# Kernel optimization log

Hardware: AMD Instinct MI355X
Metric: run time of the kernel (lower is better)

## Reference

```python
import jax, jax.numpy as jnp
import numpy as np

N_SAMPLES = 4_000_000
N_BUCKETS = 16
K_BASE = 32
K_ADJ = 16


def setup_inputs() -> dict:
    key = jax.random.key(0)
    ks = jax.random.split(key, 8)
    return {
        "x": jax.random.uniform(ks[0], (N_SAMPLES,), dtype=jnp.float32),
        "x_mins": jnp.zeros((N_BUCKETS,), jnp.float32),
        "x_maxs": jnp.ones((N_BUCKETS,), jnp.float32),
        "clip_los": jnp.zeros((N_BUCKETS,), jnp.float32),
        "clip_his": jnp.ones((N_BUCKETS,), jnp.float32),
        "base_knots": jax.random.uniform(ks[1], (K_BASE,), dtype=jnp.float32),
        "base_raw_w": jax.random.normal(ks[2], (K_BASE,), dtype=jnp.float32),
        "base_bias": jax.random.normal(ks[3], (1,), dtype=jnp.float32),
        "adj_knots": jax.random.uniform(ks[4], (K_ADJ,), dtype=jnp.float32),
        "adj_raw_w": jax.random.normal(ks[5], (N_BUCKETS, K_ADJ), dtype=jnp.float32),
        "adj_bias": jax.random.normal(ks[6], (N_BUCKETS,), dtype=jnp.float32),
        "bucket_idx": jax.random.randint(ks[7], (N_SAMPLES,), 0, N_BUCKETS, dtype=jnp.int64),
    }


def _clip_and_scale(x, x_min, x_max, clip_lo, clip_hi):
    # per-sample clip (NaN clip bound => no clipping), then scale to [0,1]
    xc = jnp.where(jnp.isfinite(clip_lo), jnp.maximum(x, clip_lo), x)
    xc = jnp.where(jnp.isfinite(clip_hi), jnp.minimum(xc, clip_hi), xc)
    return jnp.clip((xc - x_min) / (x_max - x_min + 1e-12), 0.0, 1.0)


def _concave_hinge(x01, knots, raw_w, bias):
    # concave, monotone-increasing piecewise-linear spline:
    # f(x) = bias + sum_k softplus(raw_w_k) * min(x, knot_k)
    w = jax.nn.softplus(raw_w)                      # nonneg slopes -> concave increasing
    basis = jnp.minimum(x01[:, None], knots)        # [N, K]
    return bias + jnp.sum(basis * w, axis=-1)       # [N] (w may be [N,K] for per-bucket)


def reference(x, x_mins, x_maxs, clip_los, clip_his, base_knots, base_raw_w,
              base_bias, adj_knots, adj_raw_w, adj_bias, bucket_idx):
    b = bucket_idx.reshape(-1)
    xf = x.reshape(-1)
    # gather per-sample bucket scaling params (replaces the python bucket loop)
    x01 = _clip_and_scale(xf, x_mins[b], x_maxs[b], clip_los[b], clip_his[b])  # [N]
    base = _concave_hinge(x01, base_knots, base_raw_w, base_bias[0])           # [N]
    # vectorized gather-compute in place of unique()+mask dispatch
    adj = _concave_hinge(x01, adj_knots, adj_raw_w[b], adj_bias[b])            # [N]
    return (base + adj)[:, None]                                               # [N,1]
```

## Files before the change

### kernel.cpp

```cpp
#include <hip/hip_runtime.h>
#include <math.h>

#define NB 16
#define KB 32
#define KA 16
#define G  128
#define GP1 (G + 1)
#define LUT_E (NB * GP1)
#define ITERS 4


__device__ __forceinline__ float softplus_f(float v) {
    return fmaxf(v, 0.0f) + log1pf(expf(-fabsf(v)));
}

__global__ __launch_bounds__(256) void build_lut_kernel(
    const float* __restrict__ x_mins,
    const float* __restrict__ x_maxs,
    const float* __restrict__ clip_los,
    const float* __restrict__ clip_his,
    const float* __restrict__ base_knots,
    const float* __restrict__ base_raw_w,
    const float* __restrict__ base_bias,
    const float* __restrict__ adj_knots,
    const float* __restrict__ adj_raw_w,
    const float* __restrict__ adj_bias,
    float* __restrict__ ws)
{
    __shared__ float s_bw[KB], s_bk[KB], s_aw[KA], s_ak[KA];
    __shared__ float s_x0[NB], s_x1[NB];
    __shared__ float s_prm[4];
    __shared__ float s_f[GP1];

    const int tid = threadIdx.x;
    const int b   = blockIdx.x;

    if (tid < KB) { s_bw[tid] = softplus_f(base_raw_w[tid]); s_bk[tid] = base_knots[tid]; }
    if (tid < KA) { s_aw[tid] = softplus_f(adj_raw_w[b * KA + tid]); s_ak[tid] = adj_knots[tid]; }
    if (tid < NB) {
        const float mn = x_mins[tid], mx = x_maxs[tid];
        const float inva = mx - mn + 1e-12f;
        const float a = 1.0f / inva;
        const float c = -mn * a;
        const float lo = clip_los[tid], hi = clip_his[tid];
        const float Lb = isfinite(lo) ? fminf(fmaxf(fmaf(lo, a, c), 0.0f), 1.0f) : 0.0f;
        const float Hb = isfinite(hi) ? fmaxf(fminf(fmaf(hi, a, c), 1.0f), 0.0f) : 1.0f;
        const float x0 = fmaf(Lb, inva, mn);
        const float x1 = fmaf(Hb, inva, mn);
        s_x0[tid] = fminf(x0, x1);
        s_x1[tid] = fmaxf(x0, x1);
        if (tid == b) { s_prm[0] = a; s_prm[1] = c; s_prm[2] = Lb; s_prm[3] = Hb; }
    }
    __syncthreads();

    float xlo = s_x0[0], xhi = s_x1[0];
    #pragma unroll
    for (int i = 1; i < NB; ++i) { xlo = fminf(xlo, s_x0[i]); xhi = fmaxf(xhi, s_x1[i]); }
    if (!(xhi > xlo)) xhi = xlo + 1.0f;
    const float ginv  = (float)G / (xhi - xlo);
    const float hstep = (xhi - xlo) * (1.0f / (float)G);

    if (b == 0 && tid == 0) {
        ws[0] = xlo; ws[1] = ginv; ws[2] = xhi; ws[3] = xlo * ginv;
    }

    if (tid < GP1) {
        const float xj = fmaf(hstep, (float)tid, xlo);
        const float v = fminf(fmaxf(fmaf(xj, s_prm[0], s_prm[1]), s_prm[2]), s_prm[3]);
        float f = adj_bias[b] + base_bias[0];
        #pragma unroll 8
        for (int k = 0; k < KB; ++k)
            f = fmaf(s_bw[k], fminf(v, s_bk[k]), f);
        #pragma unroll 8
        for (int k = 0; k < KA; ++k)
            f = fmaf(s_aw[k], fminf(v, s_ak[k]), f);
        s_f[tid] = f;
    }
    __syncthreads();

    if (tid < GP1) {
        const int jc = min(tid, G - 1);
        const float fl = s_f[jc], fr = s_f[jc + 1];
        const float c1 = (fr - fl) * ginv;
        const float xj = fmaf(hstep, (float)jc, xlo);
        const float c0 = fmaf(-c1, xj, fl);
        ((float2*)(ws + 64))[b * GP1 + tid] = make_float2(c0, c1);
    }
}

__global__ __launch_bounds__(256) void BucketAdjustedHinge_kernel(
    const float* __restrict__ x,
    const int*   __restrict__ bucket_idx,
    const float* __restrict__ ws,
    float*       __restrict__ out,
    int n)
{
    __shared__ float2 s_lut[LUT_E];

    const int tid = threadIdx.x;
    const int gsz = gridDim.x * blockDim.x;
    const int t   = blockIdx.x * blockDim.x + tid;
    const int n4  = n >> 2;

    const float4* __restrict__ x4v = (const float4*)x;
    const int4*   __restrict__ b4v = (const int4*)bucket_idx;
    float4*       __restrict__ o4v = (float4*)out;

    float4 xa[ITERS]; int4 ba[ITERS];
    #pragma unroll
    for (int k = 0; k < ITERS; ++k) {
        const int idx = t + k * gsz;
        if (idx < n4) { xa[k] = x4v[idx]; ba[k] = b4v[idx]; }
    }

    const float xlo  = ws[0];
    const float ginv = ws[1];
    const float xhi  = ws[2];
    const float xlg  = ws[3];

    {
        const float4* __restrict__ src = (const float4*)(ws + 64);
        float4* __restrict__ dst = (float4*)s_lut;
        #pragma unroll
        for (int i = 0; i < 5; ++i) {
            const int j = tid + i * 256;
            if (j < LUT_E / 2) dst[j] = src[j];
        }
    }
    __syncthreads();

    #define EVAL1(xr, b, dstf)                                             \
        {                                                                  \
            const float xc = fminf(fmaxf((xr), xlo), xhi);                 \
            const float tt = fmaf(xc, ginv, -xlg);                         \
            const int cell = min((int)tt, G - 1);                          \
            const float2 cf = s_lut[(b) * GP1 + cell];                     \
            (dstf) = fmaf(xc, cf.y, cf.x);                                 \
        }

    #pragma unroll
    for (int k = 0; k < ITERS; ++k) {
        const int idx = t + k * gsz;
        if (idx < n4) {
            float4 r;
            EVAL1(xa[k].x, ba[k].x, r.x); EVAL1(xa[k].y, ba[k].y, r.y);
            EVAL1(xa[k].z, ba[k].z, r.z); EVAL1(xa[k].w, ba[k].w, r.w);
            o4v[idx] = r;
        }
    }

    for (int idx = t + ITERS * gsz; idx < n4; idx += gsz) {
        const float4 xv = x4v[idx];
        const int4   bv = b4v[idx];
        float4 r;
        EVAL1(xv.x, bv.x, r.x); EVAL1(xv.y, bv.y, r.y);
        EVAL1(xv.z, bv.z, r.z); EVAL1(xv.w, bv.w, r.w);
        o4v[idx] = r;
    }
    for (int i = (n4 << 2) + t; i < n; i += gsz) {
        float r;
        EVAL1(x[i], bucket_idx[i], r);
        out[i] = r;
    }
    #undef EVAL1
}

extern "C" void kernel_launch(void* const* d_in, const int* in_sizes, int n_in,
                              void* d_out, int out_size, void* d_ws, size_t ws_size,
                              hipStream_t stream) {
    const float* x          = (const float*)d_in[0];
    const float* x_mins     = (const float*)d_in[1];
    const float* x_maxs     = (const float*)d_in[2];
    const float* clip_los   = (const float*)d_in[3];
    const float* clip_his   = (const float*)d_in[4];
    const float* base_knots = (const float*)d_in[5];
    const float* base_raw_w = (const float*)d_in[6];
    const float* base_bias  = (const float*)d_in[7];
    const float* adj_knots  = (const float*)d_in[8];
    const float* adj_raw_w  = (const float*)d_in[9];
    const float* adj_bias   = (const float*)d_in[10];
    const int*   bucket_idx = (const int*)d_in[11];
    float* out = (float*)d_out;
    float* ws  = (float*)d_ws;

    const int n = in_sizes[0];

    build_lut_kernel<<<NB, 256, 0, stream>>>(
        x_mins, x_maxs, clip_los, clip_his,
        base_knots, base_raw_w, base_bias,
        adj_knots, adj_raw_w, adj_bias, ws);

    const int blocks = 1024;
    BucketAdjustedHinge_kernel<<<blocks, 256, 0, stream>>>(
        x, bucket_idx, ws, out, n);
}
```

Baseline: 18.10 us.

## Read LUT directly from global memory, use nontemporal streaming, double grid size

Drops the per-block copy of the 16x129 coefficient table into shared memory and its barrier, so lookups read a power-of-two-strided table in global memory (served by cache). Input and output streams use nontemporal loads and stores to avoid polluting cache. The grid doubles to 2048 blocks and ITERS drops to 2, trading per-thread prefetch depth for more resident waves. The risk is that random gathers from global or L1 are slower than LDS lookups.

```diff
diff --git a/kernel.cpp b/kernel.cpp
--- a/kernel.cpp
+++ b/kernel.cpp
@@ -6,8 +6,11 @@
 #define KA 16
 #define G  128
 #define GP1 (G + 1)
-#define LUT_E (NB * GP1)
-#define ITERS 4
+#define ITERS 2
+
+typedef float f4v __attribute__((ext_vector_type(4)));
+typedef int   i4v __attribute__((ext_vector_type(4)));
+typedef float f2v __attribute__((ext_vector_type(2)));
 
 
 __device__ __forceinline__ float softplus_f(float v) {
@@ -78,13 +81,12 @@
     }
     __syncthreads();
 
-    if (tid < GP1) {
-        const int jc = min(tid, G - 1);
-        const float fl = s_f[jc], fr = s_f[jc + 1];
+    if (tid < G) {
+        const float fl = s_f[tid], fr = s_f[tid + 1];
         const float c1 = (fr - fl) * ginv;
-        const float xj = fmaf(hstep, (float)jc, xlo);
+        const float xj = fmaf(hstep, (float)tid, xlo);
         const float c0 = fmaf(-c1, xj, fl);
-        ((float2*)(ws + 64))[b * GP1 + tid] = make_float2(c0, c1);
+        ((f2v*)(ws + 64))[(b << 7) | tid] = (f2v){c0, c1};
     }
 }
 
@@ -95,46 +97,37 @@
     float*       __restrict__ out,
     int n)
 {
-    __shared__ float2 s_lut[LUT_E];
-
     const int tid = threadIdx.x;
     const int gsz = gridDim.x * blockDim.x;
     const int t   = blockIdx.x * blockDim.x + tid;
     const int n4  = n >> 2;
 
-    const float4* __restrict__ x4v = (const float4*)x;
-    const int4*   __restrict__ b4v = (const int4*)bucket_idx;
-    float4*       __restrict__ o4v = (float4*)out;
-
-    float4 xa[ITERS]; int4 ba[ITERS];
-    #pragma unroll
-    for (int k = 0; k < ITERS; ++k) {
-        const int idx = t + k * gsz;
-        if (idx < n4) { xa[k] = x4v[idx]; ba[k] = b4v[idx]; }
-    }
+    const f4v* __restrict__ x4v = (const f4v*)x;
+    const i4v* __restrict__ b4v = (const i4v*)bucket_idx;
+    f4v*       __restrict__ o4v = (f4v*)out;
+    const f2v* __restrict__ lut = (const f2v*)(ws + 64);
 
     const float xlo  = ws[0];
     const float ginv = ws[1];
     const float xhi  = ws[2];
     const float xlg  = ws[3];
 
-    {
-        const float4* __restrict__ src = (const float4*)(ws + 64);
-        float4* __restrict__ dst = (float4*)s_lut;
-        #pragma unroll
-        for (int i = 0; i < 5; ++i) {
-            const int j = tid + i * 256;
-            if (j < LUT_E / 2) dst[j] = src[j];
+    f4v xa[ITERS]; i4v ba[ITERS];
+    #pragma unroll
+    for (int k = 0; k < ITERS; ++k) {
+        const int idx = t + k * gsz;
+        if (idx < n4) {
+            xa[k] = __builtin_nontemporal_load(x4v + idx);
+            ba[k] = __builtin_nontemporal_load(b4v + idx);
         }
     }
-    __syncthreads();
 
     #define EVAL1(xr, b, dstf)                                             \
         {                                                                  \
             const float xc = fminf(fmaxf((xr), xlo), xhi);                 \
             const float tt = fmaf(xc, ginv, -xlg);                         \
             const int cell = min((int)tt, G - 1);                          \
-            const float2 cf = s_lut[(b) * GP1 + cell];                     \
+            const f2v cf = lut[((b) << 7) | cell];                         \
             (dstf) = fmaf(xc, cf.y, cf.x);                                 \
         }
 
@@ -142,20 +135,20 @@
     for (int k = 0; k < ITERS; ++k) {
         const int idx = t + k * gsz;
         if (idx < n4) {
-            float4 r;
+            f4v r;
             EVAL1(xa[k].x, ba[k].x, r.x); EVAL1(xa[k].y, ba[k].y, r.y);
             EVAL1(xa[k].z, ba[k].z, r.z); EVAL1(xa[k].w, ba[k].w, r.w);
-            o4v[idx] = r;
+            __builtin_nontemporal_store(r, o4v + idx);
         }
     }
 
     for (int idx = t + ITERS * gsz; idx < n4; idx += gsz) {
-        const float4 xv = x4v[idx];
-        const int4   bv = b4v[idx];
-        float4 r;
+        const f4v xv = __builtin_nontemporal_load(x4v + idx);
+        const i4v bv = __builtin_nontemporal_load(b4v + idx);
+        f4v r;
         EVAL1(xv.x, bv.x, r.x); EVAL1(xv.y, bv.y, r.y);
         EVAL1(xv.z, bv.z, r.z); EVAL1(xv.w, bv.w, r.w);
-        o4v[idx] = r;
+        __builtin_nontemporal_store(r, o4v + idx);
     }
     for (int i = (n4 << 2) + t; i < n; i += gsz) {
         float r;
@@ -190,7 +183,7 @@
         base_knots, base_raw_w, base_bias,
         adj_knots, adj_raw_w, adj_bias, ws);
 
-    const int blocks = 1024;
+    const int blocks = 2048;
     BucketAdjustedHinge_kernel<<<blocks, 256, 0, stream>>>(
         x, bucket_idx, ws, out, n);
 }
```

New measurement: 19.92 us. 1.1x slower.
